# Optimization experiments

Measured on AMD Instinct MI355X. Metric: run time of the kernel, lower is better.

Reference implementation:

```python
import jax, jax.numpy as jnp
import numpy as np

B, N, L, E, H, D = 2, 2048, 2048, 512, 8, 3
C = E // H
ALPHA_Q = 10.0

def _ln(v, g, b):
    m = jnp.mean(v, -1, keepdims=True)
    var = jnp.mean((v - m) ** 2, -1, keepdims=True)
    return (v - m) * jax.lax.rsqrt(var + 1e-5) * g + b

def setup_inputs() -> dict:
    key = jax.random.key(0)
    ks = jax.random.split(key, 16)
    def nrm(k, shape):
        return jax.random.normal(k, shape, jnp.float32) * 0.02
    return dict(
        x=jax.random.normal(ks[0], (B, N, E), jnp.float32),
        xp=jax.random.normal(ks[1], (B, N, D), jnp.float32),
        y=jax.random.normal(ks[2], (B, L, E), jnp.float32),
        yp=jax.random.normal(ks[3], (B, L, D), jnp.float32),
        attn_mask=jnp.ones((B, 1, N, L), jnp.float32),
        pW1=jax.random.uniform(ks[4], (E, D), jnp.float32, -1.0 / D, 1.0 / D),
        pb1=jax.random.uniform(ks[5], (E,), jnp.float32, 0.0, np.pi),
        pW2=jax.random.uniform(ks[6], (E, D), jnp.float32, -1.0 / D, 1.0 / D),
        pb2=jax.random.uniform(ks[7], (E,), jnp.float32, 0.0, np.pi),
        qn_g=jnp.ones((E,), jnp.float32), qn_b=jnp.zeros((E,), jnp.float32),
        qW1=nrm(ks[8], (E, E)), qb1=jnp.zeros((E,), jnp.float32),
        qW2=nrm(ks[9], (E, E)), qb2=jnp.zeros((E,), jnp.float32),
        kn_g=jnp.ones((E,), jnp.float32), kn_b=jnp.zeros((E,), jnp.float32),
        kW1=nrm(ks[10], (E, E)), kb1=jnp.zeros((E,), jnp.float32),
        vn_g=jnp.ones((E,), jnp.float32), vn_b=jnp.zeros((E,), jnp.float32),
        vW=nrm(ks[11], (E, E)), vb=jnp.zeros((E,), jnp.float32),
        p1W=nrm(ks[12], (E, E)), p1b=jnp.zeros((E,), jnp.float32),
        p2W=nrm(ks[13], (E, D * H)), p2b=jnp.zeros((E,), jnp.float32),
    )

def reference(x, xp, y, yp, attn_mask, pW1, pb1, pW2, pb2,
              qn_g, qn_b, qW1, qb1, qW2, qb2, kn_g, kn_b, kW1, kb1,
              vn_g, vn_b, vW, vb, p1W, p1b, p2W, p2b):
    # PositionEncoder: query side with bias, key side without
    pxs = ALPHA_Q * xp
    px1 = pxs @ pW1.T + pb1
    px2 = pxs @ pW2.T + pb2
    xc1, xs1, xc2, xs2 = jnp.cos(px1), jnp.sin(px1), jnp.cos(px2), jnp.sin(px2)
    pys = ALPHA_Q * yp
    py1 = pys @ pW1.T
    py2 = pys @ pW2.T
    yc1, ys1, yc2, ys2 = jnp.cos(py1), jnp.sin(py1), jnp.cos(py2), jnp.sin(py2)

    def split(t):  # [B,S,E] -> [B,S,H,C]
        return t.reshape(t.shape[0], t.shape[1], H, C)

    # QueryEncoder
    xn = _ln(x, qn_g, qn_b)
    x1 = xn @ qW1.T + qb1
    x2 = xn @ qW2.T + qb2
    q = jnp.concatenate([split(x1 * xc1), split(x1 * xs1),
                         split(x2 * xc2), split(x2 * xs2)], -1)  # [B,N,H,4C]
    q = q.transpose(0, 2, 1, 3)  # [B,H,N,4C]
    # KeyEncoder
    yn = _ln(y, kn_g, kn_b)
    y1 = yn @ kW1.T + kb1
    k = jnp.concatenate([split(y1 * yc1), split(y1 * ys1),
                         split(yc2), split(ys2)], -1).transpose(0, 2, 1, 3)

    scale = (4 * C) ** -0.5
    attn = jax.nn.softmax(jnp.einsum('bhnd,bhld->bhnl', q, k) * scale, axis=-1)
    # custom mask renormalization
    attn = attn * attn_mask
    eps = min(1e-8, 1.0 / L)
    attn = attn / (jnp.sum(attn, -1, keepdims=True) + eps)

    v = (_ln(y, vn_g, vn_b) @ vW.T + vb).reshape(B, L, H, C).transpose(0, 2, 1, 3)
    out1 = jnp.einsum('bhnl,bhlc->bhnc', attn, v).transpose(0, 2, 1, 3).reshape(B, N, E)
    out1 = out1 @ p1W.T + p1b

    out2 = jnp.einsum('bhnl,bld->bhnd', attn, yp) - xp[:, None]  # [B,H,N,D]
    out2 = out2.transpose(0, 2, 1, 3).reshape(B, N, H * D) @ p2W.T + p2b
    return (out1 + out2, attn)
```

## Files before the change

### kernel.cpp

```cpp
#include <hip/hip_runtime.h>

typedef unsigned short ushort_t;
typedef __attribute__((ext_vector_type(8))) __bf16 bf16x8;
typedef __attribute__((ext_vector_type(4))) float f32x4;

__device__ __forceinline__ f32x4 mfma16(bf16x8 a, bf16x8 b, f32x4 c) {
  return __builtin_amdgcn_mfma_f32_16x16x32_bf16(a, b, c, 0, 0, 0);
}

__device__ __forceinline__ ushort_t f2bf(float f) {
  unsigned int x = __float_as_uint(f);
  unsigned int r = (x + 0x7fffu + ((x >> 16) & 1u)) >> 16;
  return (ushort_t)r;
}

static constexpr size_t SZ_XN   = 4096ull * 512 * 2;
static constexpr size_t SZ_W    = 512ull * 512 * 2;
static constexpr size_t OFS_XN   = 0;
static constexpr size_t OFS_YNK  = OFS_XN + SZ_XN;
static constexpr size_t OFS_YNV  = OFS_YNK + SZ_XN;
static constexpr size_t OFS_WQ12 = OFS_YNV + SZ_XN;
static constexpr size_t OFS_WK1  = OFS_WQ12 + 2 * SZ_W;
static constexpr size_t OFS_WV   = OFS_WK1 + SZ_W;
static constexpr size_t OFS_WP1  = OFS_WV + SZ_W;
static constexpr size_t OFS_QB12 = OFS_WP1 + SZ_W;
static constexpr size_t OFS_FLAG = OFS_QB12 + 4096;
static constexpr size_t OFS_X12  = OFS_FLAG + 256;
static constexpr size_t OFS_Y1   = OFS_X12 + 4096ull * 1024 * 4;
static constexpr size_t OFS_VV   = OFS_Y1 + 4096ull * 512 * 4;
static constexpr size_t OFS_Q    = OFS_VV + 4096ull * 512 * 4;
static constexpr size_t OFS_K    = OFS_Q + 16ull * 2048 * 256 * 2;
static constexpr size_t OFS_VT   = OFS_K + 16ull * 2048 * 256 * 2;
static constexpr size_t OFS_O1   = OFS_VT + 16ull * 80 * 2048 * 2;
static constexpr size_t OFS_O2   = OFS_O1 + 4096ull * 512 * 2;

__global__ void k_convert(const float* __restrict__ qW1, const float* __restrict__ qW2,
                          const float* __restrict__ kW1, const float* __restrict__ vW,
                          const float* __restrict__ p1W,
                          const float* __restrict__ qb1, const float* __restrict__ qb2,
                          ushort_t* wq12, ushort_t* wk1, ushort_t* wv, ushort_t* wp1,
                          float* qb12, int* flag) {
  int seg = blockIdx.y;
  int idx = blockIdx.x * 256 + threadIdx.x;
  switch (seg) {
    case 0: wq12[idx] = f2bf(qW1[idx]);
            if (idx < 512) qb12[idx] = qb1[idx];
            if (idx == 0) *flag = 1;
            break;
    case 1: wq12[262144 + idx] = f2bf(qW2[idx]);
            if (idx < 512) qb12[512 + idx] = qb2[idx];
            break;
    case 2: wk1[idx] = f2bf(kW1[idx]); break;
    case 3: wv[idx]  = f2bf(vW[idx]);  break;
    case 4: wp1[idx] = f2bf(p1W[idx]); break;
  }
}

__global__ void k_maskchk(const float4* __restrict__ mask, int* flag, int n4) {
  int i = blockIdx.x * blockDim.x + threadIdx.x;
  bool bad = false;
  for (; i < n4; i += gridDim.x * blockDim.x) {
    float4 v = mask[i];
    bad |= (v.x != 1.f) | (v.y != 1.f) | (v.z != 1.f) | (v.w != 1.f);
  }
  if (bad) atomicAnd(flag, 0);
}

__global__ __launch_bounds__(256) void k_ln1(const float* __restrict__ x,
                                             const float* __restrict__ g, const float* __restrict__ b,
                                             ushort_t* __restrict__ out) {
  int row = blockIdx.x, tid = threadIdx.x;
  const float* xr = x + (size_t)row * 512;
  float v0 = xr[tid], v1 = xr[tid + 256];
  float s = v0 + v1, q = v0 * v0 + v1 * v1;
  for (int m = 32; m; m >>= 1) { s += __shfl_xor(s, m, 64); q += __shfl_xor(q, m, 64); }
  __shared__ float ls[8];
  int wid = tid >> 6, lane = tid & 63;
  if (lane == 0) { ls[wid] = s; ls[4 + wid] = q; }
  __syncthreads();
  s = ls[0] + ls[1] + ls[2] + ls[3];
  q = ls[4] + ls[5] + ls[6] + ls[7];
  float mean = s * (1.f / 512), var = q * (1.f / 512) - mean * mean;
  float rs = rsqrtf(var + 1e-5f);
  ushort_t* o = out + (size_t)row * 512;
  o[tid]       = f2bf((v0 - mean) * rs * g[tid] + b[tid]);
  o[tid + 256] = f2bf((v1 - mean) * rs * g[tid + 256] + b[tid + 256]);
}

__global__ __launch_bounds__(256) void k_ln2(const float* __restrict__ y,
                                             const float* __restrict__ g1, const float* __restrict__ b1,
                                             const float* __restrict__ g2, const float* __restrict__ b2,
                                             ushort_t* __restrict__ o1, ushort_t* __restrict__ o2) {
  int row = blockIdx.x, tid = threadIdx.x;
  const float* yr = y + (size_t)row * 512;
  float v0 = yr[tid], v1 = yr[tid + 256];
  float s = v0 + v1, q = v0 * v0 + v1 * v1;
  for (int m = 32; m; m >>= 1) { s += __shfl_xor(s, m, 64); q += __shfl_xor(q, m, 64); }
  __shared__ float ls[8];
  int wid = tid >> 6, lane = tid & 63;
  if (lane == 0) { ls[wid] = s; ls[4 + wid] = q; }
  __syncthreads();
  s = ls[0] + ls[1] + ls[2] + ls[3];
  q = ls[4] + ls[5] + ls[6] + ls[7];
  float mean = s * (1.f / 512), var = q * (1.f / 512) - mean * mean;
  float rs = rsqrtf(var + 1e-5f);
  float t0 = (v0 - mean) * rs, t1 = (v1 - mean) * rs;
  ushort_t* p1 = o1 + (size_t)row * 512;
  ushort_t* p2 = o2 + (size_t)row * 512;
  p1[tid]       = f2bf(t0 * g1[tid] + b1[tid]);
  p1[tid + 256] = f2bf(t1 * g1[tid + 256] + b1[tid + 256]);
  p2[tid]       = f2bf(t0 * g2[tid] + b2[tid]);
  p2[tid + 256] = f2bf(t1 * g2[tid + 256] + b2[tid + 256]);
}

__global__ __launch_bounds__(256) void k_gemm(const ushort_t* __restrict__ A, const ushort_t* __restrict__ W,
                                              const float* __restrict__ bias, float* __restrict__ Cmat,
                                              int M, int Nn, int K, int mode,
                                              const float* __restrict__ o2, const float* __restrict__ p2W,
                                              const float* __restrict__ p2b) {
  __shared__ __align__(16) ushort_t lA[128 * 40];
  __shared__ __align__(16) ushort_t lB[128 * 40];
  int tid = threadIdx.x;
  int wid = tid >> 6, lane = tid & 63, lg = lane >> 4, lc = lane & 15;
  int m0 = blockIdx.y * 128, n0 = blockIdx.x * 128;
  int wm = wid >> 1, wn = wid & 1;
  f32x4 acc[4][4];
#pragma unroll
  for (int i = 0; i < 4; i++)
#pragma unroll
    for (int j = 0; j < 4; j++) acc[i][j] = (f32x4){0, 0, 0, 0};

  for (int k0 = 0; k0 < K; k0 += 32) {
    __syncthreads();
#pragma unroll
    for (int i = 0; i < 2; i++) {
      int u = tid + i * 256;
      int row = u >> 2, off = u & 3;
      *(int4*)(&lA[row * 40 + off * 8]) = *(const int4*)(A + (size_t)(m0 + row) * K + k0 + off * 8);
      *(int4*)(&lB[row * 40 + off * 8]) = *(const int4*)(W + (size_t)(n0 + row) * K + k0 + off * 8);
    }
    __syncthreads();
    bf16x8 af[4], bf[4];
#pragma unroll
    for (int mt = 0; mt < 4; mt++) af[mt] = *(const bf16x8*)(&lA[(wm * 64 + mt * 16 + lc) * 40 + lg * 8]);
#pragma unroll
    for (int nt = 0; nt < 4; nt++) bf[nt] = *(const bf16x8*)(&lB[(wn * 64 + nt * 16 + lc) * 40 + lg * 8]);
#pragma unroll
    for (int mt = 0; mt < 4; mt++)
#pragma unroll
      for (int nt = 0; nt < 4; nt++) acc[mt][nt] = mfma16(af[mt], bf[nt], acc[mt][nt]);
  }

#pragma unroll
  for (int mt = 0; mt < 4; mt++) {
#pragma unroll
    for (int nt = 0; nt < 4; nt++) {
      int col = n0 + wn * 64 + nt * 16 + lc;
      float bcol = bias[col];
#pragma unroll
      for (int r = 0; r < 4; r++) {
        int row = m0 + wm * 64 + mt * 16 + lg * 4 + r;
        float v = acc[mt][nt][r] + bcol;
        if (mode == 1) {
          const float* o2r = o2 + (size_t)row * 24;
          const float* wr = p2W + (size_t)col * 24;
          float sdot = p2b[col];
#pragma unroll
          for (int j = 0; j < 24; j++) sdot += o2r[j] * wr[j];
          v += sdot;
        }
        Cmat[(size_t)row * Nn + col] = v;
      }
    }
  }
}

__global__ __launch_bounds__(256) void k_scatter_q(const float* __restrict__ x12, const float* __restrict__ xp,
                                                   const float* __restrict__ pW1, const float* __restrict__ pb1,
                                                   const float* __restrict__ pW2, const float* __restrict__ pb2,
                                                   ushort_t* __restrict__ q) {
  int rown = blockIdx.x;
  int b = rown >> 11, n = rown & 2047;
  float p0 = xp[(size_t)rown * 3] * 10.f;
  float p1 = xp[(size_t)rown * 3 + 1] * 10.f;
  float p2v = xp[(size_t)rown * 3 + 2] * 10.f;
  const float* x1r = x12 + (size_t)rown * 1024;
#pragma unroll
  for (int i = 0; i < 2; i++) {
    int e = threadIdx.x + i * 256;
    float a1 = p0 * pW1[e * 3] + p1 * pW1[e * 3 + 1] + p2v * pW1[e * 3 + 2] + pb1[e];
    float a2 = p0 * pW2[e * 3] + p1 * pW2[e * 3 + 1] + p2v * pW2[e * 3 + 2] + pb2[e];
    float c1, s1, c2, s2;
    __sincosf(a1, &s1, &c1);
    __sincosf(a2, &s2, &c2);
    float x1 = x1r[e], x2 = x1r[512 + e];
    int h = e >> 6, c = e & 63;
    ushort_t* qr = q + (((size_t)b * 8 + h) * 2048 + n) * 256;
    qr[c]       = f2bf(x1 * c1);
    qr[64 + c]  = f2bf(x1 * s1);
    qr[128 + c] = f2bf(x2 * c2);
    qr[192 + c] = f2bf(x2 * s2);
  }
}

__global__ __launch_bounds__(256) void k_scatter_k(const float* __restrict__ y1, const float* __restrict__ yp,
                                                   const float* __restrict__ pW1, const float* __restrict__ pW2,
                                                   ushort_t* __restrict__ kk) {
  int rown = blockIdx.x;
  int b = rown >> 11, n = rown & 2047;
  float p0 = yp[(size_t)rown * 3] * 10.f;
  float p1 = yp[(size_t)rown * 3 + 1] * 10.f;
  float p2v = yp[(size_t)rown * 3 + 2] * 10.f;
  const float* y1r = y1 + (size_t)rown * 512;
#pragma unroll
  for (int i = 0; i < 2; i++) {
    int e = threadIdx.x + i * 256;
    float a1 = p0 * pW1[e * 3] + p1 * pW1[e * 3 + 1] + p2v * pW1[e * 3 + 2];
    float a2 = p0 * pW2[e * 3] + p1 * pW2[e * 3 + 1] + p2v * pW2[e * 3 + 2];
    float c1, s1, c2, s2;
    __sincosf(a1, &s1, &c1);
    __sincosf(a2, &s2, &c2);
    float v1 = y1r[e];
    int h = e >> 6, c = e & 63;
    ushort_t* kr = kk + (((size_t)b * 8 + h) * 2048 + n) * 256;
    kr[c]       = f2bf(v1 * c1);
    kr[64 + c]  = f2bf(v1 * s1);
    kr[128 + c] = f2bf(c2);
    kr[192 + c] = f2bf(s2);
  }
}

__global__ void k_vt(const float* __restrict__ vv, ushort_t* __restrict__ vt) {
  int l0 = blockIdx.x * 64, h = blockIdx.y, b = blockIdx.z;
  __shared__ ushort_t t[64][66];
  int tx = threadIdx.x, ty = threadIdx.y;
#pragma unroll
  for (int i = 0; i < 16; i++) {
    int lr = i * 4 + ty;
    t[lr][tx] = f2bf(vv[((size_t)(b * 2048 + l0 + lr)) * 512 + h * 64 + tx]);
  }
  __syncthreads();
#pragma unroll
  for (int i = 0; i < 16; i++) {
    int col = i * 4 + ty;
    vt[(((size_t)b * 8 + h) * 80 + col) * 2048 + l0 + tx] = t[tx][col];
  }
}

__global__ void k_vt_extra(const float* __restrict__ yp, ushort_t* __restrict__ vt) {
  int l = blockIdx.x * 256 + threadIdx.x;
  int j = blockIdx.y, bh = blockIdx.z;
  int b = bh >> 3;
  ushort_t v = 0;
  if (j < 3) v = f2bf(yp[((size_t)b * 2048 + l) * 3 + j]);
  vt[((size_t)bh * 80 + 64 + j) * 2048 + l] = v;
}

__global__ __launch_bounds__(256, 2) void k_attn(const ushort_t* __restrict__ qbuf,
                                                 const ushort_t* __restrict__ kbuf,
                                                 const ushort_t* __restrict__ vt,
                                                 const float* __restrict__ mask, const int* __restrict__ flag,
                                                 const float* __restrict__ xp,
                                                 float* __restrict__ attn_out, ushort_t* __restrict__ o1,
                                                 float* __restrict__ o2) {
  __shared__ __align__(16) ushort_t kT[64 * 264];
  __shared__ __align__(16) ushort_t vT[80 * 72];
  __shared__ __align__(16) ushort_t aT[4 * 16 * 72];
  int h = blockIdx.y, b = blockIdx.z;
  int bh = b * 8 + h;
  int tid = threadIdx.x, wid = tid >> 6, lane = tid & 63, lg = lane >> 4, lc = lane & 15;
  int n0 = blockIdx.x * 64;
  int wrow = n0 + wid * 16;
  const bool ones = (*flag != 0);

  bf16x8 qf[8];
  {
    const ushort_t* qr = qbuf + ((size_t)bh * 2048 + wrow + lc) * 256 + lg * 8;
#pragma unroll
    for (int ks = 0; ks < 8; ks++) qf[ks] = *(const bf16x8*)(qr + ks * 32);
  }
  float rs0[4] = {0, 0, 0, 0}, rs1[4] = {0, 0, 0, 0};

  for (int l0 = 0; l0 < 2048; l0 += 64) {
    __syncthreads();
#pragma unroll
    for (int i = 0; i < 8; i++) {
      int u = tid + i * 256;
      int row = u >> 5, off = u & 31;
      *(int4*)(&kT[row * 264 + off * 8]) =
          *(const int4*)(kbuf + ((size_t)bh * 2048 + l0 + row) * 256 + off * 8);
    }
    __syncthreads();
    f32x4 sacc[4];
#pragma unroll
    for (int nt = 0; nt < 4; nt++) sacc[nt] = (f32x4){0, 0, 0, 0};
#pragma unroll
    for (int ks = 0; ks < 8; ks++)
#pragma unroll
      for (int nt = 0; nt < 4; nt++) {
        bf16x8 kf = *(const bf16x8*)(&kT[(nt * 16 + lc) * 264 + ks * 32 + lg * 8]);
        sacc[nt] = mfma16(qf[ks], kf, sacc[nt]);
      }
    float pr0[4] = {0, 0, 0, 0}, pr1[4] = {0, 0, 0, 0};
#pragma unroll
    for (int nt = 0; nt < 4; nt++)
#pragma unroll
      for (int r = 0; r < 4; r++) {
        float T = __expf(sacc[nt][r] * 0.0625f);
        pr0[r] += T;
        if (!ones) {
          float m = mask[((size_t)b * 2048 + wrow + lg * 4 + r) * 2048 + l0 + nt * 16 + lc];
          pr1[r] += T * m;
        }
      }
#pragma unroll
    for (int r = 0; r < 4; r++) {
#pragma unroll
      for (int s2 = 1; s2 < 16; s2 <<= 1) {
        pr0[r] += __shfl_xor(pr0[r], s2, 64);
        if (!ones) pr1[r] += __shfl_xor(pr1[r], s2, 64);
      }
      rs0[r] += pr0[r];
      rs1[r] += ones ? pr0[r] : pr1[r];
    }
  }
  float inv[4];
#pragma unroll
  for (int r = 0; r < 4; r++) inv[r] = 1.f / (rs1[r] + 1e-8f * rs0[r]);

  f32x4 pacc[5];
#pragma unroll
  for (int nt = 0; nt < 5; nt++) pacc[nt] = (f32x4){0, 0, 0, 0};

  for (int l0 = 0; l0 < 2048; l0 += 64) {
    __syncthreads();
#pragma unroll
    for (int i = 0; i < 8; i++) {
      int u = tid + i * 256;
      int row = u >> 5, off = u & 31;
      *(int4*)(&kT[row * 264 + off * 8]) =
          *(const int4*)(kbuf + ((size_t)bh * 2048 + l0 + row) * 256 + off * 8);
    }
#pragma unroll
    for (int i = 0; i < 3; i++) {
      int u = tid + i * 256;
      if (u < 640) {
        int row = u >> 3, off = u & 7;
        *(int4*)(&vT[row * 72 + off * 8]) =
            *(const int4*)(vt + ((size_t)bh * 80 + row) * 2048 + l0 + off * 8);
      }
    }
    __syncthreads();
    f32x4 sacc[4];
#pragma unroll
    for (int nt = 0; nt < 4; nt++) sacc[nt] = (f32x4){0, 0, 0, 0};
#pragma unroll
    for (int ks = 0; ks < 8; ks++)
#pragma unroll
      for (int nt = 0; nt < 4; nt++) {
        bf16x8 kf = *(const bf16x8*)(&kT[(nt * 16 + lc) * 264 + ks * 32 + lg * 8]);
        sacc[nt] = mfma16(qf[ks], kf, sacc[nt]);
      }
#pragma unroll
    for (int nt = 0; nt < 4; nt++)
#pragma unroll
      for (int r = 0; r < 4; r++) {
        float T = __expf(sacc[nt][r] * 0.0625f);
        float m = 1.f;
        if (!ones) m = mask[((size_t)b * 2048 + wrow + lg * 4 + r) * 2048 + l0 + nt * 16 + lc];
        float a = T * m * inv[r];
        attn_out[((size_t)bh * 2048 + wrow + lg * 4 + r) * 2048 + l0 + nt * 16 + lc] = a;
        aT[wid * 1152 + (lg * 4 + r) * 72 + nt * 16 + lc] = f2bf(a);
      }
    asm volatile("s_waitcnt lgkmcnt(0)" ::: "memory");
#pragma unroll
    for (int ks = 0; ks < 2; ks++) {
      bf16x8 af = *(const bf16x8*)(&aT[wid * 1152 + lc * 72 + ks * 32 + lg * 8]);
#pragma unroll
      for (int nt = 0; nt < 5; nt++) {
        bf16x8 vf = *(const bf16x8*)(&vT[(nt * 16 + lc) * 72 + ks * 32 + lg * 8]);
        pacc[nt] = mfma16(af, vf, pacc[nt]);
      }
    }
  }

#pragma unroll
  for (int nt = 0; nt < 4; nt++)
#pragma unroll
    for (int r = 0; r < 4; r++) {
      int n = wrow + lg * 4 + r;
      o1[((size_t)b * 2048 + n) * 512 + h * 64 + nt * 16 + lc] = f2bf(pacc[nt][r]);
    }
  if (lc < 3) {
#pragma unroll
    for (int r = 0; r < 4; r++) {
      int n = wrow + lg * 4 + r;
      o2[((size_t)b * 2048 + n) * 24 + h * 3 + lc] = pacc[4][r] - xp[((size_t)b * 2048 + n) * 3 + lc];
    }
  }
}

extern "C" void kernel_launch(void* const* d_in, const int* in_sizes, int n_in,
                              void* d_out, int out_size, void* d_ws, size_t ws_size,
                              hipStream_t stream) {
  const float* x    = (const float*)d_in[0];
  const float* xp   = (const float*)d_in[1];
  const float* y    = (const float*)d_in[2];
  const float* yp   = (const float*)d_in[3];
  const float* mask = (const float*)d_in[4];
  const float* pW1  = (const float*)d_in[5];
  const float* pb1  = (const float*)d_in[6];
  const float* pW2  = (const float*)d_in[7];
  const float* pb2  = (const float*)d_in[8];
  const float* qn_g = (const float*)d_in[9];
  const float* qn_b = (const float*)d_in[10];
  const float* qW1  = (const float*)d_in[11];
  const float* qb1  = (const float*)d_in[12];
  const float* qW2  = (const float*)d_in[13];
  const float* qb2  = (const float*)d_in[14];
  const float* kn_g = (const float*)d_in[15];
  const float* kn_b = (const float*)d_in[16];
  const float* kW1  = (const float*)d_in[17];
  const float* kb1  = (const float*)d_in[18];
  const float* vn_g = (const float*)d_in[19];
  const float* vn_b = (const float*)d_in[20];
  const float* vW   = (const float*)d_in[21];
  const float* vb   = (const float*)d_in[22];
  const float* p1W  = (const float*)d_in[23];
  const float* p1b  = (const float*)d_in[24];
  const float* p2W  = (const float*)d_in[25];
  const float* p2b  = (const float*)d_in[26];

  char* ws = (char*)d_ws;
  ushort_t* xn   = (ushort_t*)(ws + OFS_XN);
  ushort_t* ynk  = (ushort_t*)(ws + OFS_YNK);
  ushort_t* ynv  = (ushort_t*)(ws + OFS_YNV);
  ushort_t* wq12 = (ushort_t*)(ws + OFS_WQ12);
  ushort_t* wk1  = (ushort_t*)(ws + OFS_WK1);
  ushort_t* wv   = (ushort_t*)(ws + OFS_WV);
  ushort_t* wp1  = (ushort_t*)(ws + OFS_WP1);
  float*    qb12 = (float*)(ws + OFS_QB12);
  int*      flag = (int*)(ws + OFS_FLAG);
  float*    x12  = (float*)(ws + OFS_X12);
  float*    y1b  = (float*)(ws + OFS_Y1);
  float*    vvb  = (float*)(ws + OFS_VV);
  ushort_t* qb   = (ushort_t*)(ws + OFS_Q);
  ushort_t* kb   = (ushort_t*)(ws + OFS_K);
  ushort_t* vtb  = (ushort_t*)(ws + OFS_VT);
  ushort_t* o1   = (ushort_t*)(ws + OFS_O1);
  float*    o2   = (float*)(ws + OFS_O2);

  float* out0 = (float*)d_out;
  float* attn_out = (float*)d_out + 2097152;

  k_convert<<<dim3(1024, 5), 256, 0, stream>>>(qW1, qW2, kW1, vW, p1W, qb1, qb2,
                                               wq12, wk1, wv, wp1, qb12, flag);
  k_maskchk<<<2048, 256, 0, stream>>>((const float4*)mask, flag, 2097152);
  k_ln1<<<4096, 256, 0, stream>>>(x, qn_g, qn_b, xn);
  k_ln2<<<4096, 256, 0, stream>>>(y, kn_g, kn_b, vn_g, vn_b, ynk, ynv);
  k_gemm<<<dim3(8, 32), 256, 0, stream>>>(xn, wq12, qb12, x12, 4096, 1024, 512, 0, nullptr, nullptr, nullptr);
  k_gemm<<<dim3(4, 32), 256, 0, stream>>>(ynk, wk1, kb1, y1b, 4096, 512, 512, 0, nullptr, nullptr, nullptr);
  k_gemm<<<dim3(4, 32), 256, 0, stream>>>(ynv, wv, vb, vvb, 4096, 512, 512, 0, nullptr, nullptr, nullptr);
  k_scatter_q<<<4096, 256, 0, stream>>>(x12, xp, pW1, pb1, pW2, pb2, qb);
  k_scatter_k<<<4096, 256, 0, stream>>>(y1b, yp, pW1, pW2, kb);
  k_vt<<<dim3(32, 8, 2), dim3(64, 4), 0, stream>>>(vvb, vtb);
  k_vt_extra<<<dim3(8, 16, 16), 256, 0, stream>>>(yp, vtb);
  k_attn<<<dim3(32, 8, 2), 256, 0, stream>>>(qb, kb, vtb, mask, flag, xp, attn_out, o1, o2);
  k_gemm<<<dim3(4, 32), 256, 0, stream>>>(o1, wp1, p1b, out0, 4096, 512, 512, 1, o2, p2W, p2b);
}
```

Measured before the change: 396.2 us.

## Double-buffer K tiles via global_load_lds with swizzle, stream V from global

Reworks the attention kernel to load K in 32-row tiles directly into LDS through global_load_lds, double-buffered so the next tile loads while the current one computes. The LDS layout is XOR-swizzled in place of padding. V fragments are now read straight from global memory rather than staged in LDS. The attention output is written with nontemporal stores, row-sum reductions are deferred to after the loop, and the grid is flattened so heads of the same row block sit next to each other. The risks are the vmcnt wait accounting mixing direct V loads with the async K stages, and more global traffic for V.

```diff
diff --git a/kernel.cpp b/kernel.cpp
--- a/kernel.cpp
+++ b/kernel.cpp
@@ -259,19 +259,25 @@
 __global__ __launch_bounds__(256, 2) void k_attn(const ushort_t* __restrict__ qbuf,
                                                  const ushort_t* __restrict__ kbuf,
                                                  const ushort_t* __restrict__ vt,
-                                                 const float* __restrict__ mask, const int* __restrict__ flag,
+                                                 const float* __restrict__ mask,
+                                                 const int* __restrict__ flag,
                                                  const float* __restrict__ xp,
-                                                 float* __restrict__ attn_out, ushort_t* __restrict__ o1,
+                                                 float* __restrict__ attn_out,
+                                                 ushort_t* __restrict__ o1,
                                                  float* __restrict__ o2) {
-  __shared__ __align__(16) ushort_t kT[64 * 264];
-  __shared__ __align__(16) ushort_t vT[80 * 72];
-  __shared__ __align__(16) ushort_t aT[4 * 16 * 72];
-  int h = blockIdx.y, b = blockIdx.z;
-  int bh = b * 8 + h;
+  __shared__ __align__(16) ushort_t kL[2][32 * 256];
+  __shared__ __align__(16) ushort_t aT[4][16][40];
+
+  int flat = blockIdx.x;
+  int bh = flat & 15, rb = flat >> 4;
+  int b = bh >> 3, h = bh & 7;
   int tid = threadIdx.x, wid = tid >> 6, lane = tid & 63, lg = lane >> 4, lc = lane & 15;
-  int n0 = blockIdx.x * 64;
+  int n0 = rb * 64;
   int wrow = n0 + wid * 16;
   const bool ones = (*flag != 0);
+
+  const ushort_t* Kb = kbuf + (size_t)bh * 2048 * 256;
+  const ushort_t* Vb = vt + (size_t)bh * 80 * 2048;
 
   bf16x8 qf[8];
   {
@@ -279,110 +285,123 @@
 #pragma unroll
     for (int ks = 0; ks < 8; ks++) qf[ks] = *(const bf16x8*)(qr + ks * 32);
   }
-  float rs0[4] = {0, 0, 0, 0}, rs1[4] = {0, 0, 0, 0};
-
-  for (int l0 = 0; l0 < 2048; l0 += 64) {
-    __syncthreads();
-#pragma unroll
-    for (int i = 0; i < 8; i++) {
-      int u = tid + i * 256;
-      int row = u >> 5, off = u & 31;
-      *(int4*)(&kT[row * 264 + off * 8]) =
-          *(const int4*)(kbuf + ((size_t)bh * 2048 + l0 + row) * 256 + off * 8);
-    }
-    __syncthreads();
-    f32x4 sacc[4];
-#pragma unroll
-    for (int nt = 0; nt < 4; nt++) sacc[nt] = (f32x4){0, 0, 0, 0};
-#pragma unroll
-    for (int ks = 0; ks < 8; ks++)
-#pragma unroll
-      for (int nt = 0; nt < 4; nt++) {
-        bf16x8 kf = *(const bf16x8*)(&kT[(nt * 16 + lc) * 264 + ks * 32 + lg * 8]);
-        sacc[nt] = mfma16(qf[ks], kf, sacc[nt]);
-      }
-    float pr0[4] = {0, 0, 0, 0}, pr1[4] = {0, 0, 0, 0};
-#pragma unroll
-    for (int nt = 0; nt < 4; nt++)
+
+  int sg_src[4], sg_dst[4];
+#pragma unroll
+  for (int i = 0; i < 4; i++) {
+    int g = wid * 256 + i * 64 + lane;
+    int row = g >> 5;
+    int gc = (g & 31) ^ (row & 7);
+    sg_src[i] = row * 256 + gc * 8;
+    sg_dst[i] = (wid * 256 + i * 64) * 8;
+  }
+
+#define STAGE(s, t)                                                                     \
+  {                                                                                     \
+    const ushort_t* tb = Kb + (size_t)(t) * 32 * 256;                                   \
+    _Pragma("unroll")                                                                   \
+    for (int i = 0; i < 4; i++) {                                                       \
+      __builtin_amdgcn_global_load_lds(                                                 \
+          (const __attribute__((address_space(1))) void*)(tb + sg_src[i]),              \
+          (__attribute__((address_space(3))) void*)(&kL[s][sg_dst[i]]), 16, 0, 0);      \
+    }                                                                                   \
+  }
+
+  int r3 = (lc & 7);
+
+  float rsE[4] = {0, 0, 0, 0}, rsM[4] = {0, 0, 0, 0};
+  STAGE(0, 0);
+  asm volatile("s_waitcnt vmcnt(0)" ::: "memory");
+  __syncthreads();
+  for (int t = 0; t < 64; t++) {
+    int s = t & 1;
+    if (t < 63) { STAGE(s ^ 1, t + 1); }
+    __builtin_amdgcn_sched_barrier(0);
+    f32x4 sacc[2];
+    sacc[0] = (f32x4){0, 0, 0, 0};
+    sacc[1] = (f32x4){0, 0, 0, 0};
+#pragma unroll
+    for (int ks = 0; ks < 8; ks++) {
+      int gb = ((ks * 4 + lg) ^ r3) * 8;
+      bf16x8 k0 = *(const bf16x8*)(&kL[s][lc * 256 + gb]);
+      bf16x8 k1 = *(const bf16x8*)(&kL[s][(16 + lc) * 256 + gb]);
+      sacc[0] = mfma16(qf[ks], k0, sacc[0]);
+      sacc[1] = mfma16(qf[ks], k1, sacc[1]);
+    }
+#pragma unroll
+    for (int nt = 0; nt < 2; nt++)
 #pragma unroll
       for (int r = 0; r < 4; r++) {
         float T = __expf(sacc[nt][r] * 0.0625f);
-        pr0[r] += T;
+        rsE[r] += T;
         if (!ones) {
-          float m = mask[((size_t)b * 2048 + wrow + lg * 4 + r) * 2048 + l0 + nt * 16 + lc];
-          pr1[r] += T * m;
+          float m = mask[((size_t)b * 2048 + wrow + lg * 4 + r) * 2048 + t * 32 + nt * 16 + lc];
+          rsM[r] += T * m;
         }
       }
-#pragma unroll
-    for (int r = 0; r < 4; r++) {
-#pragma unroll
-      for (int s2 = 1; s2 < 16; s2 <<= 1) {
-        pr0[r] += __shfl_xor(pr0[r], s2, 64);
-        if (!ones) pr1[r] += __shfl_xor(pr1[r], s2, 64);
-      }
-      rs0[r] += pr0[r];
-      rs1[r] += ones ? pr0[r] : pr1[r];
-    }
-  }
+    asm volatile("s_waitcnt vmcnt(0)" ::: "memory");
+    __syncthreads();
+  }
+
   float inv[4];
 #pragma unroll
-  for (int r = 0; r < 4; r++) inv[r] = 1.f / (rs1[r] + 1e-8f * rs0[r]);
+  for (int r = 0; r < 4; r++) {
+#pragma unroll
+    for (int s2 = 1; s2 < 16; s2 <<= 1) {
+      rsE[r] += __shfl_xor(rsE[r], s2, 64);
+      if (!ones) rsM[r] += __shfl_xor(rsM[r], s2, 64);
+    }
+    float denom = (ones ? rsE[r] : rsM[r]) + 1e-8f * rsE[r];
+    inv[r] = 1.f / denom;
+  }
 
   f32x4 pacc[5];
 #pragma unroll
   for (int nt = 0; nt < 5; nt++) pacc[nt] = (f32x4){0, 0, 0, 0};
 
-  for (int l0 = 0; l0 < 2048; l0 += 64) {
-    __syncthreads();
-#pragma unroll
-    for (int i = 0; i < 8; i++) {
-      int u = tid + i * 256;
-      int row = u >> 5, off = u & 31;
-      *(int4*)(&kT[row * 264 + off * 8]) =
-          *(const int4*)(kbuf + ((size_t)bh * 2048 + l0 + row) * 256 + off * 8);
-    }
-#pragma unroll
-    for (int i = 0; i < 3; i++) {
-      int u = tid + i * 256;
-      if (u < 640) {
-        int row = u >> 3, off = u & 7;
-        *(int4*)(&vT[row * 72 + off * 8]) =
-            *(const int4*)(vt + ((size_t)bh * 80 + row) * 2048 + l0 + off * 8);
-      }
-    }
-    __syncthreads();
-    f32x4 sacc[4];
-#pragma unroll
-    for (int nt = 0; nt < 4; nt++) sacc[nt] = (f32x4){0, 0, 0, 0};
-#pragma unroll
-    for (int ks = 0; ks < 8; ks++)
-#pragma unroll
-      for (int nt = 0; nt < 4; nt++) {
-        bf16x8 kf = *(const bf16x8*)(&kT[(nt * 16 + lc) * 264 + ks * 32 + lg * 8]);
-        sacc[nt] = mfma16(qf[ks], kf, sacc[nt]);
-      }
-#pragma unroll
-    for (int nt = 0; nt < 4; nt++)
+  STAGE(0, 0);
+  asm volatile("s_waitcnt vmcnt(0)" ::: "memory");
+  __syncthreads();
+  for (int t = 0; t < 64; t++) {
+    int s = t & 1;
+    if (t < 63) { STAGE(s ^ 1, t + 1); }
+    __builtin_amdgcn_sched_barrier(0);
+    int l0 = t * 32;
+    f32x4 sacc[2];
+    sacc[0] = (f32x4){0, 0, 0, 0};
+    sacc[1] = (f32x4){0, 0, 0, 0};
+#pragma unroll
+    for (int ks = 0; ks < 8; ks++) {
+      int gb = ((ks * 4 + lg) ^ r3) * 8;
+      bf16x8 k0 = *(const bf16x8*)(&kL[s][lc * 256 + gb]);
+      bf16x8 k1 = *(const bf16x8*)(&kL[s][(16 + lc) * 256 + gb]);
+      sacc[0] = mfma16(qf[ks], k0, sacc[0]);
+      sacc[1] = mfma16(qf[ks], k1, sacc[1]);
+    }
+#pragma unroll
+    for (int nt = 0; nt < 2; nt++)
 #pragma unroll
       for (int r = 0; r < 4; r++) {
         float T = __expf(sacc[nt][r] * 0.0625f);
         float m = 1.f;
         if (!ones) m = mask[((size_t)b * 2048 + wrow + lg * 4 + r) * 2048 + l0 + nt * 16 + lc];
         float a = T * m * inv[r];
-        attn_out[((size_t)bh * 2048 + wrow + lg * 4 + r) * 2048 + l0 + nt * 16 + lc] = a;
-        aT[wid * 1152 + (lg * 4 + r) * 72 + nt * 16 + lc] = f2bf(a);
+        __builtin_nontemporal_store(
+            a, &attn_out[((size_t)bh * 2048 + wrow + lg * 4 + r) * 2048 + l0 + nt * 16 + lc]);
+        aT[wid][lg * 4 + r][nt * 16 + lc] = f2bf(a);
       }
     asm volatile("s_waitcnt lgkmcnt(0)" ::: "memory");
-#pragma unroll
-    for (int ks = 0; ks < 2; ks++) {
-      bf16x8 af = *(const bf16x8*)(&aT[wid * 1152 + lc * 72 + ks * 32 + lg * 8]);
-#pragma unroll
-      for (int nt = 0; nt < 5; nt++) {
-        bf16x8 vf = *(const bf16x8*)(&vT[(nt * 16 + lc) * 72 + ks * 32 + lg * 8]);
-        pacc[nt] = mfma16(af, vf, pacc[nt]);
-      }
-    }
-  }
+    __builtin_amdgcn_sched_barrier(0);
+    bf16x8 af = *(const bf16x8*)(&aT[wid][lc][lg * 8]);
+#pragma unroll
+    for (int nt = 0; nt < 5; nt++) {
+      bf16x8 vf = *(const bf16x8*)(Vb + (size_t)(nt * 16 + lc) * 2048 + l0 + lg * 8);
+      pacc[nt] = mfma16(af, vf, pacc[nt]);
+    }
+    asm volatile("s_waitcnt vmcnt(8)" ::: "memory");
+    __syncthreads();
+  }
+#undef STAGE
 
 #pragma unroll
   for (int nt = 0; nt < 4; nt++)
@@ -465,6 +484,6 @@
   k_scatter_k<<<4096, 256, 0, stream>>>(y1b, yp, pW1, pW2, kb);
   k_vt<<<dim3(32, 8, 2), dim3(64, 4), 0, stream>>>(vvb, vtb);
   k_vt_extra<<<dim3(8, 16, 16), 256, 0, stream>>>(yp, vtb);
-  k_attn<<<dim3(32, 8, 2), 256, 0, stream>>>(qb, kb, vtb, mask, flag, xp, attn_out, o1, o2);
+  k_attn<<<dim3(512), 256, 0, stream>>>(qb, kb, vtb, mask, flag, xp, attn_out, o1, o2);
   k_gemm<<<dim3(4, 32), 256, 0, stream>>>(o1, wp1, p1b, out0, 4096, 512, 512, 1, o2, p2W, p2b);
 }
```

Result: faster. 362.1 us (-8.6%).
